# Performance work log

Measured on AMD Instinct MI355X. Metric: run time of the kernel, lower is better.

Reference implementation:

```python
import jax, jax.numpy as jnp
import numpy as np

B, P, H, D1, D2 = 8, 96, 96, 128, 128


def setup_inputs() -> dict:
    key = jax.random.key(0)
    k1, k2, k3 = jax.random.split(key, 3)
    premise = jax.random.normal(k1, (B, P, D1), dtype=jnp.float32)
    hypothesis = jax.random.normal(k2, (B, H, D2), dtype=jnp.float32)
    # lecun_normal-ish scale: std = 1/sqrt(fan_in) with fan_in = D1*D2
    kernel = jax.random.normal(k3, (P, H, D1, D2), dtype=jnp.float32) / np.sqrt(D1 * D2)
    return {"premise": premise, "hypothesis": hypothesis, "kernel": kernel}


def reference(premise, hypothesis, kernel):
    # ret[b,p,h] = sum_{i,j} premise[b,p,i] * kernel[p,h,i,j] * hypothesis[b,h,j]
    # Fused contraction; avoids the 5D broadcasted intermediates of the original.
    return jnp.einsum('bpi,phij,bhj->bph', premise, kernel, hypothesis)
```

## Files before the change

kernel.cpp:

```cpp
#include <hip/hip_runtime.h>
#include <hip/hip_bf16.h>
#include <stdint.h>

#define NB 8
#define NP 96
#define NH 96
#define ND 128

__global__ __launch_bounds__(256) void interaction_kernel(
    const float* __restrict__ prem,
    const float* __restrict__ hyp,
    const float* __restrict__ kern,
    float* __restrict__ out)
{
    const int h = blockIdx.x;
    const int p = blockIdx.y;
    const int t = threadIdx.x;

    __shared__ float ldsP[ND * NB];
    __shared__ float ldsH[NB * ND];
    __shared__ float ldsR[4 * NB];

    {
        const int b = t & 7, c = t >> 3;
        const float4 v = *(const float4*)(prem + ((size_t)(b * NP + p)) * ND + c * 4);
        const int i0 = c * 4;
        ldsP[(i0 + 0) * NB + b] = v.x;
        ldsP[(i0 + 1) * NB + b] = v.y;
        ldsP[(i0 + 2) * NB + b] = v.z;
        ldsP[(i0 + 3) * NB + b] = v.w;
        const float4 w = *(const float4*)(hyp + ((size_t)(b * NH + h)) * ND + c * 4);
        *(float4*)&ldsH[b * ND + c * 4] = w;
    }
    __syncthreads();

    const int jc = t & 31;
    const int rg = t >> 5;
    const int j0 = jc * 4;

    float hyr[NB][4];
    #pragma unroll
    for (int b = 0; b < NB; ++b) {
        const float4 w = *(const float4*)&ldsH[b * ND + j0];
        hyr[b][0] = w.x; hyr[b][1] = w.y; hyr[b][2] = w.z; hyr[b][3] = w.w;
    }

    float acc[NB];
    #pragma unroll
    for (int b = 0; b < NB; ++b) acc[b] = 0.f;

    const float4* kb4 = (const float4*)(kern + ((size_t)(p * NH + h)) * (ND * ND));

    #pragma unroll 4
    for (int r = 0; r < 16; ++r) {
        const int i = rg * 16 + r;
        const float4 kv = kb4[i * 32 + jc];

        const float4 pa = *(const float4*)&ldsP[i * NB];
        const float4 pb = *(const float4*)&ldsP[i * NB + 4];
        const float pv[8] = {pa.x, pa.y, pa.z, pa.w, pb.x, pb.y, pb.z, pb.w};

        #pragma unroll
        for (int b = 0; b < NB; ++b) {
            float s = kv.x * hyr[b][0];
            s = fmaf(kv.y, hyr[b][1], s);
            s = fmaf(kv.z, hyr[b][2], s);
            s = fmaf(kv.w, hyr[b][3], s);
            acc[b] = fmaf(pv[b], s, acc[b]);
        }
    }

    #pragma unroll
    for (int b = 0; b < NB; ++b) {
        #pragma unroll
        for (int off = 32; off > 0; off >>= 1)
            acc[b] += __shfl_down(acc[b], off, 64);
    }
    const int lane = t & 63, wave = t >> 6;
    if (lane == 0) {
        #pragma unroll
        for (int b = 0; b < NB; ++b) ldsR[wave * NB + b] = acc[b];
    }
    __syncthreads();
    if (t < NB) {
        const float s = ldsR[t] + ldsR[NB + t] + ldsR[2 * NB + t] + ldsR[3 * NB + t];
        out[(size_t)t * (NP * NH) + p * NH + h] = s;
    }
}

extern "C" void kernel_launch(void* const* d_in, const int* in_sizes, int n_in,
                              void* d_out, int out_size, void* d_ws, size_t ws_size,
                              hipStream_t stream) {
    const float* prem = (const float*)d_in[0];
    const float* hyp  = (const float*)d_in[1];
    const float* kern = (const float*)d_in[2];
    float* out = (float*)d_out;

    dim3 grid(NH, NP);
    dim3 block(256);
    interaction_kernel<<<grid, block, 0, stream>>>(prem, hyp, kern, out);
}
```

Baseline: 748.4 us.

## Process two hypothesis rows per block and batch kernel loads eight deep

Each block now handles two h indices, which halves the grid and reuses the premise tile staged in LDS for both. Kernel-tensor loads are grouped eight float4s at a time, so more global loads are in flight before the FMAs begin. A minimum-occupancy launch bound is also added. The kernel is a 600MB stream and memory-bound, so the gain depends on more memory-level parallelism. The deeper prefetch raises register pressure and may lower occupancy.

```diff
diff --git a/kernel.cpp b/kernel.cpp
--- a/kernel.cpp
+++ b/kernel.cpp
@@ -1,25 +1,25 @@
 #include <hip/hip_runtime.h>
-#include <hip/hip_bf16.h>
 #include <stdint.h>
 
 #define NB 8
 #define NP 96
 #define NH 96
 #define ND 128
+#define TH 2
 
-__global__ __launch_bounds__(256) void interaction_kernel(
+__global__ __launch_bounds__(256, 4) void interaction_kernel(
     const float* __restrict__ prem,
     const float* __restrict__ hyp,
     const float* __restrict__ kern,
     float* __restrict__ out)
 {
-    const int h = blockIdx.x;
-    const int p = blockIdx.y;
-    const int t = threadIdx.x;
+    const int h0 = blockIdx.x * TH;
+    const int p  = blockIdx.y;
+    const int t  = threadIdx.x;
 
     __shared__ float ldsP[ND * NB];
-    __shared__ float ldsH[NB * ND];
-    __shared__ float ldsR[4 * NB];
+    __shared__ float ldsH[TH][NB * ND];
+    __shared__ float ldsR[TH][4 * NB];
 
     {
         const int b = t & 7, c = t >> 3;
@@ -29,8 +29,11 @@
         ldsP[(i0 + 1) * NB + b] = v.y;
         ldsP[(i0 + 2) * NB + b] = v.z;
         ldsP[(i0 + 3) * NB + b] = v.w;
-        const float4 w = *(const float4*)(hyp + ((size_t)(b * NH + h)) * ND + c * 4);
-        *(float4*)&ldsH[b * ND + c * 4] = w;
+        #pragma unroll
+        for (int hh = 0; hh < TH; ++hh) {
+            const float4 w = *(const float4*)(hyp + ((size_t)(b * NH + h0 + hh)) * ND + c * 4);
+            *(float4*)&ldsH[hh][b * ND + c * 4] = w;
+        }
     }
     __syncthreads();
 
@@ -38,53 +41,70 @@
     const int rg = t >> 5;
     const int j0 = jc * 4;
 
-    float hyr[NB][4];
+    float acc[TH][NB];
     #pragma unroll
-    for (int b = 0; b < NB; ++b) {
-        const float4 w = *(const float4*)&ldsH[b * ND + j0];
-        hyr[b][0] = w.x; hyr[b][1] = w.y; hyr[b][2] = w.z; hyr[b][3] = w.w;
-    }
+    for (int hh = 0; hh < TH; ++hh)
+        #pragma unroll
+        for (int b = 0; b < NB; ++b) acc[hh][b] = 0.f;
 
-    float acc[NB];
     #pragma unroll
-    for (int b = 0; b < NB; ++b) acc[b] = 0.f;
+    for (int hh = 0; hh < TH; ++hh) {
+        const float4* kt = (const float4*)(kern + ((size_t)(p * NH + h0 + hh)) * (ND * ND));
 
-    const float4* kb4 = (const float4*)(kern + ((size_t)(p * NH + h)) * (ND * ND));
-
-    #pragma unroll 4
-    for (int r = 0; r < 16; ++r) {
-        const int i = rg * 16 + r;
-        const float4 kv = kb4[i * 32 + jc];
-
-        const float4 pa = *(const float4*)&ldsP[i * NB];
-        const float4 pb = *(const float4*)&ldsP[i * NB + 4];
-        const float pv[8] = {pa.x, pa.y, pa.z, pa.w, pb.x, pb.y, pb.z, pb.w};
+        float hyr[NB][4];
+        #pragma unroll
+        for (int b = 0; b < NB; ++b) {
+            const float4 w = *(const float4*)&ldsH[hh][b * ND + j0];
+            hyr[b][0] = w.x; hyr[b][1] = w.y; hyr[b][2] = w.z; hyr[b][3] = w.w;
+        }
 
         #pragma unroll
-        for (int b = 0; b < NB; ++b) {
-            float s = kv.x * hyr[b][0];
-            s = fmaf(kv.y, hyr[b][1], s);
-            s = fmaf(kv.z, hyr[b][2], s);
-            s = fmaf(kv.w, hyr[b][3], s);
-            acc[b] = fmaf(pv[b], s, acc[b]);
+        for (int half = 0; half < 2; ++half) {
+            float4 kq[8];
+            #pragma unroll
+            for (int r = 0; r < 8; ++r)
+                kq[r] = kt[(size_t)(rg * 16 + half * 8 + r) * 32 + jc];
+
+            #pragma unroll
+            for (int r = 0; r < 8; ++r) {
+                const int i = rg * 16 + half * 8 + r;
+                const float4 pa = *(const float4*)&ldsP[i * NB];
+                const float4 pb = *(const float4*)&ldsP[i * NB + 4];
+                const float pv[8] = {pa.x, pa.y, pa.z, pa.w, pb.x, pb.y, pb.z, pb.w};
+
+                #pragma unroll
+                for (int b = 0; b < NB; ++b) {
+                    float s = kq[r].x * hyr[b][0];
+                    s = fmaf(kq[r].y, hyr[b][1], s);
+                    s = fmaf(kq[r].z, hyr[b][2], s);
+                    s = fmaf(kq[r].w, hyr[b][3], s);
+                    acc[hh][b] = fmaf(pv[b], s, acc[hh][b]);
+                }
+            }
         }
     }
 
     #pragma unroll
-    for (int b = 0; b < NB; ++b) {
+    for (int hh = 0; hh < TH; ++hh)
         #pragma unroll
-        for (int off = 32; off > 0; off >>= 1)
-            acc[b] += __shfl_down(acc[b], off, 64);
-    }
+        for (int b = 0; b < NB; ++b)
+            #pragma unroll
+            for (int off = 32; off > 0; off >>= 1)
+                acc[hh][b] += __shfl_down(acc[hh][b], off, 64);
+
     const int lane = t & 63, wave = t >> 6;
     if (lane == 0) {
         #pragma unroll
-        for (int b = 0; b < NB; ++b) ldsR[wave * NB + b] = acc[b];
+        for (int hh = 0; hh < TH; ++hh)
+            #pragma unroll
+            for (int b = 0; b < NB; ++b)
+                ldsR[hh][wave * NB + b] = acc[hh][b];
     }
     __syncthreads();
-    if (t < NB) {
-        const float s = ldsR[t] + ldsR[NB + t] + ldsR[2 * NB + t] + ldsR[3 * NB + t];
-        out[(size_t)t * (NP * NH) + p * NH + h] = s;
+    if (t < NB * TH) {
+        const int b = t & 7, hh = t >> 3;
+        const float s = ldsR[hh][b] + ldsR[hh][NB + b] + ldsR[hh][2 * NB + b] + ldsR[hh][3 * NB + b];
+        out[(size_t)b * (NP * NH) + p * NH + (h0 + hh)] = s;
     }
 }
 
@@ -96,7 +116,7 @@
     const float* kern = (const float*)d_in[2];
     float* out = (float*)d_out;
 
-    dim3 grid(NH, NP);
+    dim3 grid(NH / TH, NP);
     dim3 block(256);
     interaction_kernel<<<grid, block, 0, stream>>>(prem, hyp, kern, out);
 }
```

Measured after the change: 945.2 us. 26.3% more time.
